# Optimization experiments

Hardware: AMD Instinct MI355X
Metric: run time of the kernel (lower is better)

## Reference

```python
import jax, jax.numpy as jnp
import numpy as np

# --- fixed OpenCV filter kernels ---
# cv2.getGaussianKernel(3, 1): exp(-(i-1)^2/2), normalized -> [0.27407, 0.45186, 0.27407]
_g = np.exp(-((np.arange(3) - 1.0) ** 2) / 2.0)
GAUSS_1D = (_g / _g.sum()).astype(np.float32)
# cv2 Sobel/Laplacian ksize=9 separable parts (unnormalized, as cv2.Laplacian uses):
#   smoothing = binomial row C(8,k); second derivative = C(6,k) conv [1,-2,1]
SMOOTH_9 = np.array([1, 8, 28, 56, 70, 56, 28, 8, 1], dtype=np.float32)
D2_9 = np.array([1, 4, 4, -4, -10, -4, 4, 4, 1], dtype=np.float32)


def _depthwise_conv(x, k2d):
    """Depthwise 2D correlation with BORDER_REFLECT_101 padding (cv2 default).

    x: [N,H,W,C] float, k2d: [kh,kw] float (symmetric, so corr == conv)."""
    C = x.shape[-1]
    rh, rw = k2d.shape[0] // 2, k2d.shape[1] // 2
    # jnp 'reflect' == OpenCV BORDER_REFLECT_101 (edge pixel not duplicated)
    xp = jnp.pad(x, ((0, 0), (rh, rh), (rw, rw), (0, 0)), mode='reflect')
    k = jnp.broadcast_to(k2d[:, :, None, None], (k2d.shape[0], k2d.shape[1], 1, C))
    return jax.lax.conv_general_dilated(
        xp, k, window_strides=(1, 1), padding='VALID',
        dimension_numbers=('NHWC', 'HWIO', 'NHWC'),
        feature_group_count=C)


def setup_inputs() -> dict:
    key = jax.random.key(0)
    # uint8-range image batch, as the original layer feeds uint8 data to OpenCV
    x = jax.random.uniform(key, (32, 512, 512, 3), dtype=jnp.float32) * 255.0
    return {"x": x}


def reference(x) -> jnp.ndarray:
    g = jnp.asarray(GAUSS_1D)
    blur = _depthwise_conv(x, jnp.outer(g, g))  # GaussianBlur(ksize=3, sigma=1)
    lap_k = jnp.asarray(np.outer(SMOOTH_9, D2_9) + np.outer(D2_9, SMOOTH_9))
    lap = _depthwise_conv(blur, lap_k) + 1.0  # delta = 1
    # CV_8UC1 destination depth -> saturate to [0, 255]
    return jnp.clip(lap, 0.0, 255.0)
```

## Files before the change

### kernel.cpp

```cpp
#include <hip/hip_runtime.h>


#define TH 16
#define TW 32
#define FW (TW*3)
#define BP (TW+8)
#define BFU (BP*3)
#define BF 132
#define BHR (TH+8)
#define HIMG 512
#define WIMG 512
#define ROWF (WIMG*3)

__device__ __forceinline__ int reflect101(int i, int n) {
    i = (i < 0) ? -i : i;
    return (i >= n) ? (2 * n - 2 - i) : i;
}

__device__ __forceinline__ float4 fma4(float s, const float4& a, const float4& b) {
    return make_float4(fmaf(s, a.x, b.x), fmaf(s, a.y, b.y),
                       fmaf(s, a.z, b.z), fmaf(s, a.w, b.w));
}

__global__ __launch_bounds__(256, 5)
void log_fused(const float* __restrict__ x, float* __restrict__ out) {
    __shared__ __align__(16) float blur[BHR * BF];
    __shared__ __align__(16) float t1[TH * BF];
    __shared__ __align__(16) float t2[TH * BF];

    const int tid  = threadIdx.x;
    const int col0 = blockIdx.x * TW;
    const int row0 = blockIdx.y * TH;
    const float* const xn = x + (size_t)blockIdx.z * HIMG * ROWF;

    const float G0 = 0.2740686190f, G1 = 0.4518627620f;

    if (tid < 240) {
        const int lc = tid % BFU;
        const int rg = tid / BFU;
        const int p  = lc / 3;
        const int ch = lc - 3 * p;
        const int gc = reflect101(col0 - 4 + p, WIMG);
        const int xm = reflect101(gc - 1, WIMG) * 3 + ch;
        const int x0 = gc * 3 + ch;
        const int xp = reflect101(gc + 1, WIMG) * 3 + ch;
        #pragma unroll
        for (int r = rg; r < BHR; r += 2) {
            const int g  = row0 - 4 + r;
            const int gr = reflect101(g, HIMG);
            const float* pa = xn + (size_t)reflect101(gr - 1, HIMG) * ROWF;
            const float* pb = xn + (size_t)gr * ROWF;
            const float* pc = xn + (size_t)reflect101(gr + 1, HIMG) * ROWF;
            const float h0 = G0 * (pa[xm] + pa[xp]) + G1 * pa[x0];
            const float h1 = G0 * (pb[xm] + pb[xp]) + G1 * pb[x0];
            const float h2 = G0 * (pc[xm] + pc[xp]) + G1 * pc[x0];
            blur[r * BF + lc] = G0 * (h0 + h2) + G1 * h1;
        }
    }
    __syncthreads();

    const float S9[9] = {1.f, 8.f, 28.f, 56.f, 70.f, 56.f, 28.f, 8.f, 1.f};
    const float D9[9] = {1.f, 4.f, 4.f, -4.f, -10.f, -4.f, 4.f, 4.f, 1.f};

    if (tid < 240) {
        const int rg  = tid / 30;
        const int qc  = tid - rg * 30;
        const int lr0 = rg * 2;
        const int lc  = qc * 4;
        float4 w[10];
        #pragma unroll
        for (int k = 0; k < 10; ++k)
            w[k] = *(const float4*)&blur[(lr0 + k) * BF + lc];
        float4 a1r0 = make_float4(0.f, 0.f, 0.f, 0.f), a2r0 = a1r0;
        float4 a1r1 = a1r0, a2r1 = a1r0;
        #pragma unroll
        for (int k = 0; k < 9; ++k) {
            a1r0 = fma4(S9[k], w[k],     a1r0);
            a2r0 = fma4(D9[k], w[k],     a2r0);
            a1r1 = fma4(S9[k], w[k + 1], a1r1);
            a2r1 = fma4(D9[k], w[k + 1], a2r1);
        }
        *(float4*)&t1[(lr0    ) * BF + lc] = a1r0;
        *(float4*)&t1[(lr0 + 1) * BF + lc] = a1r1;
        *(float4*)&t2[(lr0    ) * BF + lc] = a2r0;
        *(float4*)&t2[(lr0 + 1) * BF + lc] = a2r1;
    }
    __syncthreads();

    if (tid < 192) {
        const int lr = tid / 12;
        const int qp = tid - lr * 12;
        const int lc = qp * 8;
        float w1[32], w2[32];
        #pragma unroll
        for (int q = 0; q < 8; ++q) {
            float4 v = *(const float4*)&t1[lr * BF + lc + 4 * q];
            w1[4*q+0] = v.x; w1[4*q+1] = v.y; w1[4*q+2] = v.z; w1[4*q+3] = v.w;
            float4 u = *(const float4*)&t2[lr * BF + lc + 4 * q];
            w2[4*q+0] = u.x; w2[4*q+1] = u.y; w2[4*q+2] = u.z; w2[4*q+3] = u.w;
        }
        float o[8];
        #pragma unroll
        for (int j = 0; j < 8; ++j) {
            float a = 1.0f;
            #pragma unroll
            for (int k = 0; k < 9; ++k) {
                a = fmaf(D9[k], w1[j + 3 * k], a);
                a = fmaf(S9[k], w2[j + 3 * k], a);
            }
            o[j] = fminf(fmaxf(a, 0.0f), 255.0f);
        }
        float* op = out + (size_t)blockIdx.z * HIMG * ROWF
                        + (size_t)(row0 + lr) * ROWF + (size_t)(col0 * 3 + lc);
        *(float4*)&op[0] = make_float4(o[0], o[1], o[2], o[3]);
        *(float4*)&op[4] = make_float4(o[4], o[5], o[6], o[7]);
    }
}

extern "C" void kernel_launch(void* const* d_in, const int* in_sizes, int n_in,
                              void* d_out, int out_size, void* d_ws, size_t ws_size,
                              hipStream_t stream) {
    const float* x = (const float*)d_in[0];
    float* outp = (float*)d_out;
    const int nimg = in_sizes[0] / (HIMG * WIMG * 3);
    dim3 grid(WIMG / TW, HIMG / TH, nimg);
    log_fused<<<grid, dim3(256, 1, 1), 0, stream>>>(x, outp);
}
```

Before: 264.4 us.

## Fold Gaussian blur into 11-tap separable LoG filters with larger tiles

Precomputes the composition of the 3-tap Gaussian with the 9-tap smoothing and second-derivative kernels into 11-tap separable filters, removing the separate blur stage and one shared-memory pass. The horizontal pass reads input rows directly with float4 loads and writes two intermediates. A vertical pass then produces four output rows per thread with register reuse. Reflect-101 borders are handled with compile-time folded coefficient tables. Tiles grow to 32x32 with 384 threads to reduce halo overhead, at the cost of extra code paths for the edge tiles and slightly different floating-point rounding.

```diff
diff --git a/kernel.cpp b/kernel.cpp
--- a/kernel.cpp
+++ b/kernel.cpp
@@ -1,119 +1,242 @@
 #include <hip/hip_runtime.h>
 
 
-#define TH 16
-#define TW 32
-#define FW (TW*3)
-#define BP (TW+8)
-#define BFU (BP*3)
-#define BF 132
-#define BHR (TH+8)
-#define HIMG 512
-#define WIMG 512
-#define ROWF (WIMG*3)
-
-__device__ __forceinline__ int reflect101(int i, int n) {
-    i = (i < 0) ? -i : i;
-    return (i >= n) ? (2 * n - 2 - i) : i;
+#define NT    384
+#define HIMG  512
+#define ROWF  1536
+#define NQ    24
+#define LSTR  96
+#define MAXG  42
+
+__device__ constexpr float SGc[11] = {
+    0.27406861900052384f, 2.6444117140031430f, 11.562892047006810f,
+    30.192548952004191f, 52.163039333992666f, 62.326078667985332f,
+    52.163039333992666f, 30.192548952004191f, 11.562892047006810f,
+    2.6444117140031430f, 0.27406861900052384f};
+__device__ constexpr float DGc[11] = {
+    0.27406861900052384f, 1.5481372380010477f, 3.1777941429984285f,
+    1.8074510479958093f, -3.4518627619989523f, -6.7111765719937139f,
+    -3.4518627619989523f, 1.8074510479958093f, 3.1777941429984285f,
+    1.5481372380010477f, 0.27406861900052384f};
+
+struct FT_t { float s[5][10]; float d[5][10]; };
+constexpr int reflc(int i) { int a = i < 0 ? -i : i; return a >= 512 ? 1022 - a : a; }
+constexpr FT_t mkft() {
+    FT_t t{};
+    const double F9s[9] = {1,8,28,56,70,56,28,8,1};
+    const double F9d[9] = {1,4,4,-4,-10,-4,4,4,1};
+    const double A = 0.27406861900052384, B = 0.45186276199895232;
+    const double g3[3] = {A, B, A};
+    for (int p = 0; p < 5; ++p)
+        for (int m = 0; m < 10; ++m) {
+            double as = 0.0, ad = 0.0;
+            for (int j = 0; j < 9; ++j) {
+                int b = reflc(p - 4 + j);
+                for (int i = 0; i < 3; ++i)
+                    if (reflc(b - 1 + i) == m) { as += F9s[j] * g3[i]; ad += F9d[j] * g3[i]; }
+            }
+            t.s[p][m] = (float)as; t.d[p][m] = (float)ad;
+        }
+    return t;
 }
-
-__device__ __forceinline__ float4 fma4(float s, const float4& a, const float4& b) {
-    return make_float4(fmaf(s, a.x, b.x), fmaf(s, a.y, b.y),
-                       fmaf(s, a.z, b.z), fmaf(s, a.w, b.w));
-}
-
-__global__ __launch_bounds__(256, 5)
-void log_fused(const float* __restrict__ x, float* __restrict__ out) {
-    __shared__ __align__(16) float blur[BHR * BF];
-    __shared__ __align__(16) float t1[TH * BF];
-    __shared__ __align__(16) float t2[TH * BF];
+__device__ constexpr FT_t FTAB = mkft();
+
+__global__ __launch_bounds__(NT, 6)
+void log_tile(const float* __restrict__ x, float* __restrict__ out) {
+    __shared__ __align__(16) float sh[2 * MAXG * LSTR];
+    float* const hS = sh;
+    float* const hD = sh + MAXG * LSTR;
 
     const int tid  = threadIdx.x;
-    const int col0 = blockIdx.x * TW;
-    const int row0 = blockIdx.y * TH;
-    const float* const xn = x + (size_t)blockIdx.z * HIMG * ROWF;
-
-    const float G0 = 0.2740686190f, G1 = 0.4518627620f;
-
-    if (tid < 240) {
-        const int lc = tid % BFU;
-        const int rg = tid / BFU;
-        const int p  = lc / 3;
-        const int ch = lc - 3 * p;
-        const int gc = reflect101(col0 - 4 + p, WIMG);
-        const int xm = reflect101(gc - 1, WIMG) * 3 + ch;
-        const int x0 = gc * 3 + ch;
-        const int xp = reflect101(gc + 1, WIMG) * 3 + ch;
-        #pragma unroll
-        for (int r = rg; r < BHR; r += 2) {
-            const int g  = row0 - 4 + r;
-            const int gr = reflect101(g, HIMG);
-            const float* pa = xn + (size_t)reflect101(gr - 1, HIMG) * ROWF;
-            const float* pb = xn + (size_t)gr * ROWF;
-            const float* pc = xn + (size_t)reflect101(gr + 1, HIMG) * ROWF;
-            const float h0 = G0 * (pa[xm] + pa[xp]) + G1 * pa[x0];
-            const float h1 = G0 * (pb[xm] + pb[xp]) + G1 * pb[x0];
-            const float h2 = G0 * (pc[xm] + pc[xp]) + G1 * pc[x0];
-            blur[r * BF + lc] = G0 * (h0 + h2) + G1 * h1;
+    const int bx   = blockIdx.x, by = blockIdx.y;
+    const int col0 = bx * 32, r0 = by * 32;
+    const int G0   = max(0, r0 - 5);
+    const int G1   = min(HIMG - 1, r0 + 36);
+    const int nG   = G1 - G0 + 1;
+    const float* xn = x   + (size_t)blockIdx.z * (HIMG * ROWF);
+    float* on       = out + (size_t)blockIdx.z * (HIMG * ROWF);
+
+    const int q    = tid % NQ;
+    const int rsub = tid / NQ;
+    const int f0   = 4 * q;
+    const bool bl  = (bx == 0  && q < 4);
+    const bool br  = (bx == 15 && q >= 20);
+
+    for (int r = rsub; r < nG; r += 16) {
+        const float* xr = xn + (size_t)(G0 + r) * ROWF;
+        float vsv[4], vdv[4];
+        if (!bl && !br) {
+            float w[36];
+            const float4* wp = (const float4*)(xr + col0 * 3 + f0 - 16);
+            #pragma unroll
+            for (int u = 0; u < 9; ++u) {
+                float4 v = wp[u];
+                w[4*u+0] = v.x; w[4*u+1] = v.y; w[4*u+2] = v.z; w[4*u+3] = v.w;
+            }
+            #pragma unroll
+            for (int j = 0; j < 4; ++j) {
+                float c = w[j + 16];
+                float s = SGc[5] * c, d = DGc[5] * c;
+                #pragma unroll
+                for (int k = 0; k < 5; ++k) {
+                    float p = w[j + 1 + 3*k] + w[j + 31 - 3*k];
+                    s = fmaf(SGc[k], p, s);
+                    d = fmaf(DGc[k], p, d);
+                }
+                vsv[j] = s; vdv[j] = d;
+            }
+        } else if (bl) {
+            float w[32];
+            const float4* wp = (const float4*)xr;
+            #pragma unroll
+            for (int u = 0; u < 8; ++u) {
+                float4 v = wp[u];
+                w[4*u+0] = v.x; w[4*u+1] = v.y; w[4*u+2] = v.z; w[4*u+3] = v.w;
+            }
+            #pragma unroll
+            for (int j = 0; j < 4; ++j) {
+                const int f = f0 + j, p = f / 3, ch = f - 3 * p;
+                float s = 0.f, d = 0.f;
+                if (p <= 4) {
+                    #pragma unroll
+                    for (int m = 0; m < 10; ++m) {
+                        float xv = w[3*m + ch];
+                        s = fmaf(FTAB.s[p][m], xv, s);
+                        d = fmaf(FTAB.d[p][m], xv, d);
+                    }
+                } else {
+                    #pragma unroll
+                    for (int k = 0; k < 11; ++k) {
+                        float xv = w[3*k];
+                        s = fmaf(SGc[k], xv, s);
+                        d = fmaf(DGc[k], xv, d);
+                    }
+                }
+                vsv[j] = s; vdv[j] = d;
+            }
+        } else {
+            float w[32];
+            const float4* wp = (const float4*)(xr + 1504);
+            #pragma unroll
+            for (int u = 0; u < 8; ++u) {
+                float4 v = wp[u];
+                w[4*u+0] = v.x; w[4*u+1] = v.y; w[4*u+2] = v.z; w[4*u+3] = v.w;
+            }
+            #pragma unroll
+            for (int j = 0; j < 4; ++j) {
+                const int f = f0 + j, p = f / 3, ch = f - 3 * p;
+                const int pc = 480 + p;
+                float s = 0.f, d = 0.f;
+                if (pc >= 507) {
+                    const int rr = 511 - pc;
+                    #pragma unroll
+                    for (int m = 0; m < 10; ++m) {
+                        float xv = w[29 - 3*m + ch];
+                        s = fmaf(FTAB.s[rr][m], xv, s);
+                        d = fmaf(FTAB.d[rr][m], xv, d);
+                    }
+                } else {
+                    #pragma unroll
+                    for (int k = 0; k < 11; ++k) {
+                        float xv = w[1 + 3*k];
+                        s = fmaf(SGc[k], xv, s);
+                        d = fmaf(DGc[k], xv, d);
+                    }
+                }
+                vsv[j] = s; vdv[j] = d;
+            }
         }
+        *(float4*)&hS[r * LSTR + f0] = make_float4(vsv[0], vsv[1], vsv[2], vsv[3]);
+        *(float4*)&hD[r * LSTR + f0] = make_float4(vdv[0], vdv[1], vdv[2], vdv[3]);
     }
     __syncthreads();
 
-    const float S9[9] = {1.f, 8.f, 28.f, 56.f, 70.f, 56.f, 28.f, 8.f, 1.f};
-    const float D9[9] = {1.f, 4.f, 4.f, -4.f, -10.f, -4.f, 4.f, 4.f, 1.f};
-
-    if (tid < 240) {
-        const int rg  = tid / 30;
-        const int qc  = tid - rg * 30;
-        const int lr0 = rg * 2;
-        const int lc  = qc * 4;
-        float4 w[10];
-        #pragma unroll
-        for (int k = 0; k < 10; ++k)
-            w[k] = *(const float4*)&blur[(lr0 + k) * BF + lc];
-        float4 a1r0 = make_float4(0.f, 0.f, 0.f, 0.f), a2r0 = a1r0;
-        float4 a1r1 = a1r0, a2r1 = a1r0;
-        #pragma unroll
-        for (int k = 0; k < 9; ++k) {
-            a1r0 = fma4(S9[k], w[k],     a1r0);
-            a2r0 = fma4(D9[k], w[k],     a2r0);
-            a1r1 = fma4(S9[k], w[k + 1], a1r1);
-            a2r1 = fma4(D9[k], w[k + 1], a2r1);
+    if (tid < 192) {
+        const int q2 = tid % NQ, rg = tid / NQ;
+        const int lr0   = 4 * rg;
+        const int rbase = r0 + lr0;
+        const int cb    = 4 * q2;
+        float* const op0 = on + (size_t)rbase * ROWF + (size_t)(col0 * 3 + cb);
+
+        if (rbase >= 5 && rbase + 3 <= 506) {
+            float4 acc[4];
+            #pragma unroll
+            for (int i = 0; i < 4; ++i) acc[i] = make_float4(1.f, 1.f, 1.f, 1.f);
+            const int pb = rbase - 5 - G0;
+            #pragma unroll
+            for (int k = 0; k < 14; ++k) {
+                const float4 d = *(const float4*)&hD[(pb + k) * LSTR + cb];
+                const float4 s = *(const float4*)&hS[(pb + k) * LSTR + cb];
+                #pragma unroll
+                for (int i = 0; i < 4; ++i) {
+                    const int kt = k - i;
+                    if (kt >= 0 && kt <= 10) {
+                        float4 a = acc[i];
+                        a.x = fmaf(SGc[kt], d.x, a.x); a.y = fmaf(SGc[kt], d.y, a.y);
+                        a.z = fmaf(SGc[kt], d.z, a.z); a.w = fmaf(SGc[kt], d.w, a.w);
+                        a.x = fmaf(DGc[kt], s.x, a.x); a.y = fmaf(DGc[kt], s.y, a.y);
+                        a.z = fmaf(DGc[kt], s.z, a.z); a.w = fmaf(DGc[kt], s.w, a.w);
+                        acc[i] = a;
+                    }
+                }
+            }
+            #pragma unroll
+            for (int i = 0; i < 4; ++i) {
+                float4 o = acc[i];
+                o.x = fminf(fmaxf(o.x, 0.f), 255.f);
+                o.y = fminf(fmaxf(o.y, 0.f), 255.f);
+                o.z = fminf(fmaxf(o.z, 0.f), 255.f);
+                o.w = fminf(fmaxf(o.w, 0.f), 255.f);
+                *(float4*)(op0 + (size_t)i * ROWF) = o;
+            }
+        } else {
+            #pragma unroll
+            for (int i = 0; i < 4; ++i) {
+                const int r = rbase + i;
+                float4 a = make_float4(1.f, 1.f, 1.f, 1.f);
+                if (r < 5) {
+                    #pragma unroll
+                    for (int m = 0; m < 10; ++m) {
+                        const float ws = FTAB.s[r][m], wd = FTAB.d[r][m];
+                        const float4 d = *(const float4*)&hD[m * LSTR + cb];
+                        const float4 s = *(const float4*)&hS[m * LSTR + cb];
+                        a.x = fmaf(ws, d.x, a.x); a.y = fmaf(ws, d.y, a.y);
+                        a.z = fmaf(ws, d.z, a.z); a.w = fmaf(ws, d.w, a.w);
+                        a.x = fmaf(wd, s.x, a.x); a.y = fmaf(wd, s.y, a.y);
+                        a.z = fmaf(wd, s.z, a.z); a.w = fmaf(wd, s.w, a.w);
+                    }
+                } else if (r > 506) {
+                    const int rr = 511 - r;
+                    #pragma unroll
+                    for (int m = 0; m < 10; ++m) {
+                        const float ws = FTAB.s[rr][m], wd = FTAB.d[rr][m];
+                        const int pi = 36 - m;
+                        const float4 d = *(const float4*)&hD[pi * LSTR + cb];
+                        const float4 s = *(const float4*)&hS[pi * LSTR + cb];
+                        a.x = fmaf(ws, d.x, a.x); a.y = fmaf(ws, d.y, a.y);
+                        a.z = fmaf(ws, d.z, a.z); a.w = fmaf(ws, d.w, a.w);
+                        a.x = fmaf(wd, s.x, a.x); a.y = fmaf(wd, s.y, a.y);
+                        a.z = fmaf(wd, s.z, a.z); a.w = fmaf(wd, s.w, a.w);
+                    }
+                } else {
+                    const int pb = r - 5 - G0;
+                    #pragma unroll
+                    for (int k = 0; k < 11; ++k) {
+                        const float4 d = *(const float4*)&hD[(pb + k) * LSTR + cb];
+                        const float4 s = *(const float4*)&hS[(pb + k) * LSTR + cb];
+                        a.x = fmaf(SGc[k], d.x, a.x); a.y = fmaf(SGc[k], d.y, a.y);
+                        a.z = fmaf(SGc[k], d.z, a.z); a.w = fmaf(SGc[k], d.w, a.w);
+                        a.x = fmaf(DGc[k], s.x, a.x); a.y = fmaf(DGc[k], s.y, a.y);
+                        a.z = fmaf(DGc[k], s.z, a.z); a.w = fmaf(DGc[k], s.w, a.w);
+                    }
+                }
+                a.x = fminf(fmaxf(a.x, 0.f), 255.f);
+                a.y = fminf(fmaxf(a.y, 0.f), 255.f);
+                a.z = fminf(fmaxf(a.z, 0.f), 255.f);
+                a.w = fminf(fmaxf(a.w, 0.f), 255.f);
+                *(float4*)(op0 + (size_t)i * ROWF) = a;
+            }
         }
-        *(float4*)&t1[(lr0    ) * BF + lc] = a1r0;
-        *(float4*)&t1[(lr0 + 1) * BF + lc] = a1r1;
-        *(float4*)&t2[(lr0    ) * BF + lc] = a2r0;
-        *(float4*)&t2[(lr0 + 1) * BF + lc] = a2r1;
-    }
-    __syncthreads();
-
-    if (tid < 192) {
-        const int lr = tid / 12;
-        const int qp = tid - lr * 12;
-        const int lc = qp * 8;
-        float w1[32], w2[32];
-        #pragma unroll
-        for (int q = 0; q < 8; ++q) {
-            float4 v = *(const float4*)&t1[lr * BF + lc + 4 * q];
-            w1[4*q+0] = v.x; w1[4*q+1] = v.y; w1[4*q+2] = v.z; w1[4*q+3] = v.w;
-            float4 u = *(const float4*)&t2[lr * BF + lc + 4 * q];
-            w2[4*q+0] = u.x; w2[4*q+1] = u.y; w2[4*q+2] = u.z; w2[4*q+3] = u.w;
-        }
-        float o[8];
-        #pragma unroll
-        for (int j = 0; j < 8; ++j) {
-            float a = 1.0f;
-            #pragma unroll
-            for (int k = 0; k < 9; ++k) {
-                a = fmaf(D9[k], w1[j + 3 * k], a);
-                a = fmaf(S9[k], w2[j + 3 * k], a);
-            }
-            o[j] = fminf(fmaxf(a, 0.0f), 255.0f);
-        }
-        float* op = out + (size_t)blockIdx.z * HIMG * ROWF
-                        + (size_t)(row0 + lr) * ROWF + (size_t)(col0 * 3 + lc);
-        *(float4*)&op[0] = make_float4(o[0], o[1], o[2], o[3]);
-        *(float4*)&op[4] = make_float4(o[4], o[5], o[6], o[7]);
     }
 }
 
@@ -122,7 +245,7 @@
                               hipStream_t stream) {
     const float* x = (const float*)d_in[0];
     float* outp = (float*)d_out;
-    const int nimg = in_sizes[0] / (HIMG * WIMG * 3);
-    dim3 grid(WIMG / TW, HIMG / TH, nimg);
-    log_fused<<<grid, dim3(256, 1, 1), 0, stream>>>(x, outp);
+    const int nimg = in_sizes[0] / (HIMG * ROWF);
+    dim3 grid(16, 16, nimg);
+    log_tile<<<grid, dim3(NT, 1, 1), 0, stream>>>(x, outp);
 }
```

Result: slower. 636.5 us (+140.7%).
